# Kernel optimization log

Measured on AMD Instinct MI355X. Metric: run time of the kernel, lower is better.

Reference implementation:

```python
import jax, jax.numpy as jnp
from jax import lax
import numpy as np

B, C_IN, D, H, W = 1, 8, 48, 256, 320
BC = 8  # base_channels
DN = ('NCHW', 'OIHW', 'NCHW')


def setup_inputs() -> dict:
    key = jax.random.key(0)
    ks = iter(jax.random.split(key, 64))
    inp = {"volume_variance": jax.random.normal(next(ks), (B, C_IN, D, H, W), jnp.float32)}
    def add(name, o, i):
        inp[name + "_w"] = jax.random.normal(next(ks), (o, i, 3, 3), jnp.float32) * 0.1
        inp[name + "_b"] = jnp.zeros((o,), jnp.float32)
    add("conv1", 2 * BC, C_IN); add("conv2", 4 * BC, 2 * BC); add("conv3", 8 * BC, 4 * BC)
    add("up3", 4 * BC, 8 * BC); add("up2", 2 * BC, 4 * BC); add("up1", BC, 2 * BC)
    add("out", 1, BC)
    add("g1_gate", 2 * BC, C_IN + BC); add("g1_cand", BC, C_IN + BC)
    add("g2_gate", 4 * BC, 4 * BC); add("g2_cand", 2 * BC, 4 * BC)
    add("g3_gate", 8 * BC, 8 * BC); add("g3_cand", 4 * BC, 8 * BC)
    add("g4_gate", 16 * BC, 16 * BC); add("g4_cand", 8 * BC, 16 * BC)
    return inp


def _conv(x, w, b, stride=1):
    # Conv2d(k=3, padding=1)
    y = lax.conv_general_dilated(x, w, (stride, stride), [(1, 1), (1, 1)], dimension_numbers=DN)
    return y + b[None, :, None, None]


def _convT(x, w, b):
    # PyTorch ConvTranspose2d(k=3, s=2, p=1, output_padding=1) as an input-dilated conv
    y = lax.conv_general_dilated(x, w, (1, 1), [(1, 2), (1, 2)], lhs_dilation=(2, 2),
                                 dimension_numbers=DN)
    return y + b[None, :, None, None]


def _gru(x, h, wg, bg, wc, bc):
    # ConvGRUCell2: fused reset/update gates, tanh candidate, convex combine
    gates = jax.nn.sigmoid(_conv(jnp.concatenate([x, h], 1), wg, bg))
    r, u = jnp.split(gates, 2, 1)
    c = jnp.tanh(_conv(jnp.concatenate([x, r * h], 1), wc, bc))
    return u * h + (1.0 - u) * c


def reference(volume_variance, conv1_w, conv1_b, conv2_w, conv2_b, conv3_w, conv3_b,
              up3_w, up3_b, up2_w, up2_b, up1_w, up1_b, out_w, out_b,
              g1_gate_w, g1_gate_b, g1_cand_w, g1_cand_b,
              g2_gate_w, g2_gate_b, g2_cand_w, g2_cand_b,
              g3_gate_w, g3_gate_b, g3_cand_w, g3_cand_b,
              g4_gate_w, g4_gate_b, g4_cand_w, g4_cand_b):
    def step(carry, cost):
        s1, s2, s3, s4 = carry
        nc = -cost                                            # [B, C_IN, H, W]
        c1 = jax.nn.relu(_conv(nc, conv1_w, conv1_b, 2))      # [B, 2BC, H/2, W/2]
        c2 = jax.nn.relu(_conv(c1, conv2_w, conv2_b, 2))      # [B, 4BC, H/4, W/4]
        c3 = jax.nn.relu(_conv(c2, conv3_w, conv3_b, 2))      # [B, 8BC, H/8, W/8]
        r4 = _gru(c3, s4, g4_gate_w, g4_gate_b, g4_cand_w, g4_cand_b)
        u3 = jax.nn.relu(_convT(r4, up3_w, up3_b))            # [B, 4BC, H/4, W/4]
        r3 = _gru(c2, s3, g3_gate_w, g3_gate_b, g3_cand_w, g3_cand_b)
        u2 = jax.nn.relu(_convT(u3 + r3, up2_w, up2_b))       # [B, 2BC, H/2, W/2]
        r2 = _gru(c1, s2, g2_gate_w, g2_gate_b, g2_cand_w, g2_cand_b)
        u1 = jax.nn.relu(_convT(u2 + r2, up1_w, up1_b))       # [B, BC, H, W]
        r1 = _gru(nc, s1, g1_gate_w, g1_gate_b, g1_cand_w, g1_cand_b)
        # ConvTranspose2d(k=3, s=1, p=1, op=0) is exactly a 3x3 same-pad conv (reparam'd weight)
        reg = _conv(u1 + r1, out_w, out_b)                    # [B, 1, H, W]
        return (r1, r2, r3, r4), reg[:, 0]
    costs = jnp.moveaxis(volume_variance, 2, 0)               # [D, B, C_IN, H, W]
    init = (jnp.zeros((B, BC, H, W), jnp.float32),
            jnp.zeros((B, 2 * BC, H // 2, W // 2), jnp.float32),
            jnp.zeros((B, 4 * BC, H // 4, W // 4), jnp.float32),
            jnp.zeros((B, 8 * BC, H // 8, W // 8), jnp.float32))
    _, outs = lax.scan(step, init, costs)                     # outs: [D, B, H, W]
    return jnp.moveaxis(outs, 0, 1)                           # [B, D, H, W]
```

## Files before the change

kernel.cpp:

```cpp
#include <hip/hip_runtime.h>
#include <math.h>

namespace {

constexpr int H0 = 256, W0 = 320, H1 = 128, W1 = 160, H2 = 64, W2 = 80, H3 = 32, W3 = 40;
constexpr int HW0 = H0 * W0, HW1 = H1 * W1, HW2 = H2 * W2, HW3 = H3 * W3;
constexpr int DEPTH = 48;
constexpr int NCS = DEPTH * HW0;

template <int CX, int CH, int COUT, int TX, int TY, int OCPT, int CHUNK,
          bool NEGX, bool CAND, int ZC>
__device__ __forceinline__ void gru_conv(
    int bx, int by, int zg, int H, int W,
    const float* __restrict__ x, int xcs,
    const float* __restrict__ h, const float* __restrict__ rg,
    const float* __restrict__ w, const float* __restrict__ bias,
    float* __restrict__ out, float* lds) {
  constexpr int CIN = CX + CH, IH = TY + 2, IW = TX + 2;
  constexpr int NPX = TX * TY, SUBS = 256 / NPX, NOCG = COUT / OCPT;
  constexpr int GPER = NOCG / ZC, NITER = GPER / SUBS;
  static_assert(NITER * SUBS == GPER && GPER * ZC == NOCG, "cfg");
  static_assert(CHUNK * IH * IW <= 6400, "lds");
  const int x0 = bx * TX, y0 = by * TY, HW = H * W, tid = threadIdx.x;
  const int px = tid % NPX, sub = tid / NPX, tx = px % TX, ty = px / TX;
  const int gbase = zg * GPER + sub;
  float acc[NITER][OCPT];
#pragma unroll
  for (int it = 0; it < NITER; it++) {
    const int g = gbase + it * SUBS;
#pragma unroll
    for (int j = 0; j < OCPT; j++) acc[it][j] = bias[g * OCPT + j];
  }
  for (int c0 = 0; c0 < CIN; c0 += CHUNK) {
    __syncthreads();
    for (int idx = tid; idx < CHUNK * IH * IW; idx += 256) {
      int cc = idx / (IH * IW), r = idx % (IH * IW), yy = r / IW, xx = r % IW;
      int gy = y0 + yy - 1, gx = x0 + xx - 1, c = c0 + cc;
      float v = 0.f;
      if ((unsigned)gy < (unsigned)H && (unsigned)gx < (unsigned)W) {
        if (c < CX) {
          v = x[(size_t)c * xcs + gy * W + gx];
          if (NEGX) v = -v;
        } else {
          int p = (c - CX) * HW + gy * W + gx;
          v = h[p];
          if (CAND) v *= rg[p];
        }
      }
      lds[idx] = v;
    }
    __syncthreads();
    for (int c = 0; c < CHUNK; c++) {
      float v[9];
      const float* lp = lds + (c * IH + ty) * IW + tx;
#pragma unroll
      for (int ky = 0; ky < 3; ky++)
#pragma unroll
        for (int kx = 0; kx < 3; kx++) v[ky * 3 + kx] = lp[ky * IW + kx];
#pragma unroll
      for (int it = 0; it < NITER; it++) {
        const int g = __builtin_amdgcn_readfirstlane(gbase + it * SUBS);
        const float* wc = w + ((size_t)(g * OCPT) * CIN + (c0 + c)) * 9;
#pragma unroll
        for (int j = 0; j < OCPT; j++)
#pragma unroll
          for (int k = 0; k < 9; k++)
            acc[it][j] = fmaf(v[k], wc[(size_t)j * CIN * 9 + k], acc[it][j]);
      }
    }
  }
  const int opix = (y0 + ty) * W + x0 + tx;
#pragma unroll
  for (int it = 0; it < NITER; it++) {
    const int g = gbase + it * SUBS;
#pragma unroll
    for (int j = 0; j < OCPT; j++) {
      const int oc = g * OCPT + j;
      float a = acc[it][j];
      if (!CAND) {
        out[oc * HW + opix] = 1.f / (1.f + expf(-a));
      } else {
        float cd = tanhf(a);
        float u = rg[(CH + oc) * HW + opix];
        float hv = h[oc * HW + opix];
        out[oc * HW + opix] = u * hv + (1.f - u) * cd;
      }
    }
  }
}

struct GruArgs {
  const float* x; int xcs;
  const float* c1; const float* c2; const float* c3;
  const float* h1; const float* h2; const float* h3; const float* h4;
  const float* g1; const float* g2; const float* g3; const float* g4;
  const float* w1; const float* b1; const float* w2; const float* b2;
  const float* w3; const float* b3; const float* w4; const float* b4;
  float* o1; float* o2; float* o3; float* o4;
};

__global__ __launch_bounds__(256) void gates_k(GruArgs a) {
  __shared__ float lds[6400];
  const int b = blockIdx.x;
  if (b < 320) {
    gru_conv<8, 8, 16, 16, 16, 8, 16, true, false, 1>(
        b % 20, b / 20, 0, H0, W0, a.x, a.xcs, a.h1, nullptr, a.w1, a.b1, a.o1, lds);
  } else if (b < 640) {
    int l = b - 320;
    gru_conv<16, 16, 32, 16, 8, 8, 32, false, false, 2>(
        l % 10, (l / 10) % 16, l / 160, H1, W1, a.c1, HW1, a.h2, nullptr, a.w2, a.b2, a.o2, lds);
  } else if (b < 800) {
    int l = b - 640;
    gru_conv<32, 32, 64, 8, 8, 8, 64, false, false, 2>(
        l % 10, (l / 10) % 8, l / 80, H2, W2, a.c2, HW2, a.h3, nullptr, a.w3, a.b3, a.o3, lds);
  } else {
    int l = b - 800;
    gru_conv<64, 64, 128, 8, 8, 4, 64, false, false, 8>(
        l % 5, (l / 5) % 4, l / 20, H3, W3, a.c3, HW3, a.h4, nullptr, a.w4, a.b4, a.o4, lds);
  }
}

__global__ __launch_bounds__(256) void cands_k(GruArgs a) {
  __shared__ float lds[6400];
  const int b = blockIdx.x;
  if (b < 320) {
    gru_conv<8, 8, 8, 16, 16, 8, 16, true, true, 1>(
        b % 20, b / 20, 0, H0, W0, a.x, a.xcs, a.h1, a.g1, a.w1, a.b1, a.o1, lds);
  } else if (b < 480) {
    int l = b - 320;
    gru_conv<16, 16, 16, 16, 8, 8, 32, false, true, 1>(
        l % 10, l / 10, 0, H1, W1, a.c1, HW1, a.h2, a.g2, a.w2, a.b2, a.o2, lds);
  } else if (b < 560) {
    int l = b - 480;
    gru_conv<32, 32, 32, 8, 8, 8, 64, false, true, 1>(
        l % 10, l / 10, 0, H2, W2, a.c2, HW2, a.h3, a.g3, a.w3, a.b3, a.o3, lds);
  } else {
    int l = b - 560;
    gru_conv<64, 64, 64, 8, 8, 4, 64, false, true, 4>(
        l % 5, (l / 5) % 4, l / 20, H3, W3, a.c3, HW3, a.h4, a.g4, a.w4, a.b4, a.o4, lds);
  }
}

template <int CIN, int COUT, int TX, int TY, int OCPT, int ZC, bool NEG>
__global__ __launch_bounds__(256) void enc_k(
    const float* __restrict__ in, int inCS, size_t inTS, int inSlots,
    const float* __restrict__ w, const float* __restrict__ bias,
    float* __restrict__ out, size_t outTS, int outSlots,
    int inH, int inW, int outH, int outW, int t0) {
  constexpr int IH = 2 * TY + 1, IW = 2 * TX + 1;
  constexpr int NPX = TX * TY, SUBS = 256 / NPX, NOCG = COUT / OCPT;
  constexpr int GPER = NOCG / ZC, NITER = GPER / SUBS;
  static_assert(NITER * SUBS == GPER, "cfg");
  __shared__ float lds[CIN * IH * IW];
  const int z = blockIdx.z, tt = t0 + z / ZC, zg = z % ZC;
  const float* inp = in + (size_t)(tt % inSlots) * inTS;
  float* outp = out + (size_t)(tt % outSlots) * outTS;
  const int x0 = blockIdx.x * TX, y0 = blockIdx.y * TY;
  const int ix0 = 2 * x0 - 1, iy0 = 2 * y0 - 1, tid = threadIdx.x;
  for (int idx = tid; idx < CIN * IH * IW; idx += 256) {
    int c = idx / (IH * IW), r = idx % (IH * IW), yy = r / IW, xx = r % IW;
    int gy = iy0 + yy, gx = ix0 + xx;
    float v = 0.f;
    if ((unsigned)gy < (unsigned)inH && (unsigned)gx < (unsigned)inW)
      v = inp[(size_t)c * inCS + gy * inW + gx];
    lds[idx] = NEG ? -v : v;
  }
  __syncthreads();
  const int px = tid % NPX, sub = tid / NPX, tx = px % TX, ty = px / TX;
  const int gbase = zg * GPER + sub;
  float acc[NITER][OCPT];
#pragma unroll
  for (int it = 0; it < NITER; it++) {
    const int g = gbase + it * SUBS;
#pragma unroll
    for (int j = 0; j < OCPT; j++) acc[it][j] = bias[g * OCPT + j];
  }
  for (int c = 0; c < CIN; c++) {
    float v[9];
    const float* lp = lds + (c * IH + 2 * ty) * IW + 2 * tx;
#pragma unroll
    for (int ky = 0; ky < 3; ky++)
#pragma unroll
      for (int kx = 0; kx < 3; kx++) v[ky * 3 + kx] = lp[ky * IW + kx];
#pragma unroll
    for (int it = 0; it < NITER; it++) {
      const int g = __builtin_amdgcn_readfirstlane(gbase + it * SUBS);
      const float* wc = w + ((size_t)(g * OCPT) * CIN + c) * 9;
#pragma unroll
      for (int j = 0; j < OCPT; j++)
#pragma unroll
        for (int k = 0; k < 9; k++)
          acc[it][j] = fmaf(v[k], wc[(size_t)j * CIN * 9 + k], acc[it][j]);
    }
  }
  const int ox = x0 + tx, oy = y0 + ty;
#pragma unroll
  for (int it = 0; it < NITER; it++) {
    const int g = gbase + it * SUBS;
#pragma unroll
    for (int j = 0; j < OCPT; j++)
      outp[((size_t)(g * OCPT + j) * outH + oy) * outW + ox] = fmaxf(acc[it][j], 0.f);
  }
}

template <int CIN, int COUT, int OCPT, int ZC, bool SUM2>
__global__ __launch_bounds__(256) void convT_b_k(
    const float* __restrict__ inA, size_t aTS, int aSlots,
    const float* __restrict__ inB, size_t bTS, int bSlots,
    const float* __restrict__ w, const float* __restrict__ bias,
    float* __restrict__ out, size_t oTS, int oSlots,
    int inH, int inW, int t0) {
  __shared__ float lds[CIN * 81];
  const int z = blockIdx.z, tt = t0 + z / ZC, zg = z % ZC;
  const float* A = inA + (size_t)(tt % aSlots) * aTS;
  const float* Bp = inB + (size_t)(tt % bSlots) * bTS;
  float* outp = out + (size_t)(tt % oSlots) * oTS;
  const int x0 = blockIdx.x * 16, y0 = blockIdx.y * 16, ix0 = x0 / 2, iy0 = y0 / 2;
  const int HWin = inH * inW, tid = threadIdx.x;
  for (int idx = tid; idx < CIN * 81; idx += 256) {
    int c = idx / 81, r = idx % 81, yy = r / 9, xx = r % 9;
    int gy = iy0 + yy, gx = ix0 + xx;
    float v = 0.f;
    if (gy < inH && gx < inW) {
      int p = c * HWin + gy * inW + gx;
      v = A[p];
      if (SUM2) v += Bp[p];
    }
    lds[idx] = v;
  }
  __syncthreads();
  constexpr int NOCG = COUT / OCPT, GPER = NOCG / ZC, SUBS = 4, NITER = GPER / SUBS;
  static_assert(NITER * SUBS == GPER, "cfg");
  const int q = tid % 64, sub = tid / 64, qx = q % 8, qy = q / 8;
  const int outW = 2 * inW, oy = y0 + 2 * qy, ox = x0 + 2 * qx;
  const int gbase = zg * GPER + sub;
  float a00[NITER][OCPT], a01[NITER][OCPT], a10[NITER][OCPT], a11[NITER][OCPT];
#pragma unroll
  for (int it = 0; it < NITER; it++) {
    const int g = gbase + it * SUBS;
#pragma unroll
    for (int j = 0; j < OCPT; j++) {
      float bb = bias[g * OCPT + j];
      a00[it][j] = bb; a01[it][j] = bb; a10[it][j] = bb; a11[it][j] = bb;
    }
  }
  for (int c = 0; c < CIN; c++) {
    const float* ip = lds + c * 81 + qy * 9 + qx;
    const float v00 = ip[0], v01 = ip[1], v10 = ip[9], v11 = ip[10];
#pragma unroll
    for (int it = 0; it < NITER; it++) {
      const int g = __builtin_amdgcn_readfirstlane(gbase + it * SUBS);
      const float* wg = w + ((size_t)(g * OCPT) * CIN + c) * 9;
#pragma unroll
      for (int j = 0; j < OCPT; j++) {
        const float* wc = wg + (size_t)j * CIN * 9;
        a00[it][j] = fmaf(wc[4], v00, a00[it][j]);
        a01[it][j] = fmaf(wc[3], v00, a01[it][j]);
        a01[it][j] = fmaf(wc[5], v01, a01[it][j]);
        a10[it][j] = fmaf(wc[1], v00, a10[it][j]);
        a10[it][j] = fmaf(wc[7], v10, a10[it][j]);
        a11[it][j] = fmaf(wc[0], v00, a11[it][j]);
        a11[it][j] = fmaf(wc[2], v01, a11[it][j]);
        a11[it][j] = fmaf(wc[6], v10, a11[it][j]);
        a11[it][j] = fmaf(wc[8], v11, a11[it][j]);
      }
    }
  }
  const int base = oy * outW + ox;
#pragma unroll
  for (int it = 0; it < NITER; it++) {
    const int g = gbase + it * SUBS;
#pragma unroll
    for (int j = 0; j < OCPT; j++) {
      float* op = outp + (size_t)(g * OCPT + j) * (4 * HWin);
      op[base] = fmaxf(a00[it][j], 0.f);
      op[base + 1] = fmaxf(a01[it][j], 0.f);
      op[base + outW] = fmaxf(a10[it][j], 0.f);
      op[base + outW + 1] = fmaxf(a11[it][j], 0.f);
    }
  }
}

__global__ __launch_bounds__(256) void up1out_k(
    const float* __restrict__ u2, size_t u2TS, int u2S,
    const float* __restrict__ r2, size_t r2TS, int r2S,
    const float* __restrict__ r1, size_t r1TS, int r1S,
    const float* __restrict__ wT, const float* __restrict__ bT,
    const float* __restrict__ wo, const float* __restrict__ bo,
    float* __restrict__ dout, int t0) {
  __shared__ float ins[16 * 121];
  __shared__ float u1h[8 * 400];
  const int t = t0 + blockIdx.z;
  const float* U = u2 + (size_t)(t % u2S) * u2TS;
  const float* R2 = r2 + (size_t)(t % r2S) * r2TS;
  const float* R1 = r1 + (size_t)(t % r1S) * r1TS;
  const int x0 = blockIdx.x * 16, y0 = blockIdx.y * 16;
  const int ix0 = x0 / 2 - 1, iy0 = y0 / 2 - 1, tid = threadIdx.x;
  for (int idx = tid; idx < 16 * 121; idx += 256) {
    int c = idx / 121, r = idx % 121, yy = r / 11, xx = r % 11;
    int gy = iy0 + yy, gx = ix0 + xx;
    float v = 0.f;
    if ((unsigned)gy < (unsigned)H1 && (unsigned)gx < (unsigned)W1) {
      int p = c * HW1 + gy * W1 + gx;
      v = U[p] + R2[p];
    }
    ins[idx] = v;
  }
  __syncthreads();
  for (int u = tid; u < 800; u += 256) {
    int ch = u / 100, qq = u % 100, qy = qq / 10, qx = qq % 10;
    float bb = bT[ch];
    float a00 = bb, a01 = bb, a10 = bb, a11 = bb;
    const float* wb = wT + (size_t)ch * 16 * 9;
    for (int ic = 0; ic < 16; ic++) {
      const float* wc = wb + ic * 9;
      const float* ip = ins + ic * 121 + qy * 11 + qx;
      float v00 = ip[0], v01 = ip[1], v10 = ip[11], v11 = ip[12];
      a00 = fmaf(wc[4], v00, a00);
      a01 = fmaf(wc[3], v00, a01); a01 = fmaf(wc[5], v01, a01);
      a10 = fmaf(wc[1], v00, a10); a10 = fmaf(wc[7], v10, a10);
      a11 = fmaf(wc[0], v00, a11); a11 = fmaf(wc[2], v01, a11);
      a11 = fmaf(wc[6], v10, a11); a11 = fmaf(wc[8], v11, a11);
    }
    float* up = u1h + ch * 400 + (2 * qy) * 20 + 2 * qx;
    up[0] = fmaxf(a00, 0.f);  up[1] = fmaxf(a01, 0.f);
    up[20] = fmaxf(a10, 0.f); up[21] = fmaxf(a11, 0.f);
  }
  __syncthreads();
  for (int idx = tid; idx < 8 * 400; idx += 256) {
    int c = idx / 400, r = idx % 400, hy = r / 20, hx = r % 20;
    int gy = y0 - 2 + hy, gx = x0 - 2 + hx;
    if ((unsigned)gy < (unsigned)H0 && (unsigned)gx < (unsigned)W0)
      u1h[idx] += R1[c * HW0 + gy * W0 + gx];
    else
      u1h[idx] = 0.f;
  }
  __syncthreads();
  const int tx = tid % 16, ty = tid / 16;
  float acc = bo[0];
  for (int c = 0; c < 8; c++) {
    const float* up = u1h + c * 400 + (ty + 1) * 20 + tx + 1;
#pragma unroll
    for (int ky = 0; ky < 3; ky++)
#pragma unroll
      for (int kx = 0; kx < 3; kx++)
        acc = fmaf(up[ky * 20 + kx], wo[c * 9 + ky * 3 + kx], acc);
  }
  dout[(size_t)t * HW0 + (y0 + ty) * W0 + x0 + tx] = acc;
}

}

extern "C" void kernel_launch(void* const* d_in, const int* in_sizes, int n_in,
                              void* d_out, int out_size, void* d_ws, size_t ws_size,
                              hipStream_t stream) {
  const float* vol = (const float*)d_in[0];
  const float* c1w = (const float*)d_in[1];  const float* c1b = (const float*)d_in[2];
  const float* c2w = (const float*)d_in[3];  const float* c2b = (const float*)d_in[4];
  const float* c3w = (const float*)d_in[5];  const float* c3b = (const float*)d_in[6];
  const float* u3w = (const float*)d_in[7];  const float* u3b = (const float*)d_in[8];
  const float* u2w = (const float*)d_in[9];  const float* u2b = (const float*)d_in[10];
  const float* u1w = (const float*)d_in[11]; const float* u1b = (const float*)d_in[12];
  const float* ow  = (const float*)d_in[13]; const float* ob  = (const float*)d_in[14];
  const float* g1gw = (const float*)d_in[15]; const float* g1gb = (const float*)d_in[16];
  const float* g1cw = (const float*)d_in[17]; const float* g1cb = (const float*)d_in[18];
  const float* g2gw = (const float*)d_in[19]; const float* g2gb = (const float*)d_in[20];
  const float* g2cw = (const float*)d_in[21]; const float* g2cb = (const float*)d_in[22];
  const float* g3gw = (const float*)d_in[23]; const float* g3gb = (const float*)d_in[24];
  const float* g3cw = (const float*)d_in[25]; const float* g3cb = (const float*)d_in[26];
  const float* g4gw = (const float*)d_in[27]; const float* g4gb = (const float*)d_in[28];
  const float* g4cw = (const float*)d_in[29]; const float* g4cb = (const float*)d_in[30];
  float* dout = (float*)d_out;
  (void)in_sizes; (void)n_in; (void)out_size;

  const size_t r1Sz = 8 * HW0, r2Sz = 16 * HW1, r3Sz = 32 * HW2, r4Sz = 64 * HW3;
  const size_t c1Sz = 16 * HW1, c2Sz = 32 * HW2, c3Sz = 64 * HW3;
  const size_t g1Sz = 16 * HW0, g2Sz = 32 * HW1, g3Sz = 64 * HW2, g4Sz = 128 * HW3;
  const size_t ZB = 8 * HW0;
  const size_t rTot = r1Sz + r2Sz + r3Sz + r4Sz;
  const size_t cTot = c1Sz + c2Sz + c3Sz;
  const size_t gTot = g1Sz + g2Sz + g3Sz + g4Sz;
  const size_t uTot = 32 * HW2 + 16 * HW1;
  const size_t needA = (ZB + 48 * rTot + 48 * cTot + gTot) * sizeof(float);
  const size_t needB = (ZB + 2 * rTot + 48 * cTot + gTot + uTot) * sizeof(float);
  const int tier = ws_size >= needA ? 0 : (ws_size >= needB ? 1 : 2);
  const int TR = (tier == 0) ? 48 : 2;
  const int TC = (tier == 2) ? 1 : 48;

  float* ws = (float*)d_ws;
  size_t off = 0;
  auto alloc = [&](size_t n) { float* p = ws + off; off += n; return p; };
  float* zb = alloc(ZB);
  float* r1 = alloc((size_t)TR * r1Sz); float* r2 = alloc((size_t)TR * r2Sz);
  float* r3 = alloc((size_t)TR * r3Sz); float* r4 = alloc((size_t)TR * r4Sz);
  float* g1 = alloc(g1Sz); float* g2 = alloc(g2Sz);
  float* g3 = alloc(g3Sz); float* g4 = alloc(g4Sz);
  float* c1a = alloc((size_t)TC * c1Sz);
  float* c2a = alloc((size_t)TC * c2Sz);
  float* c3a = alloc((size_t)TC * c3Sz);
  float *u3a, *u2a;
  if (tier == 0) {
    u3a = c1a;
    u2a = c1a + 48 * (32 * HW2);
  } else {
    u3a = alloc(32 * HW2);
    u2a = alloc(16 * HW1);
  }

  hipMemsetAsync(zb, 0, ZB * sizeof(float), stream);

  const int TD = (tier == 0) ? 48 : 1;
  if (tier < 2) {
    enc_k<8, 16, 16, 16, 8, 1, true><<<dim3(10, 8, 48), 256, 0, stream>>>(
        vol, NCS, (size_t)HW0, 48, c1w, c1b, c1a, c1Sz, 48, H0, W0, H1, W1, 0);
    enc_k<16, 32, 16, 8, 8, 1, false><<<dim3(5, 8, 48), 256, 0, stream>>>(
        c1a, HW1, c1Sz, 48, c2w, c2b, c2a, c2Sz, 48, H1, W1, H2, W2, 0);
    enc_k<32, 64, 8, 8, 8, 2, false><<<dim3(5, 4, 96), 256, 0, stream>>>(
        c2a, HW2, c2Sz, 48, c3w, c3b, c3a, c3Sz, 48, H2, W2, H3, W3, 0);
  }

  for (int t = 0; t < DEPTH; t++) {
    if (tier == 2) {
      enc_k<8, 16, 16, 16, 8, 1, true><<<dim3(10, 8, 1), 256, 0, stream>>>(
          vol, NCS, (size_t)HW0, 48, c1w, c1b, c1a, c1Sz, 1, H0, W0, H1, W1, t);
      enc_k<16, 32, 16, 8, 8, 1, false><<<dim3(5, 8, 1), 256, 0, stream>>>(
          c1a, HW1, c1Sz, 1, c2w, c2b, c2a, c2Sz, 1, H1, W1, H2, W2, t);
      enc_k<32, 64, 8, 8, 8, 2, false><<<dim3(5, 4, 2), 256, 0, stream>>>(
          c2a, HW2, c2Sz, 1, c3w, c3b, c3a, c3Sz, 1, H2, W2, H3, W3, t);
    }
    const float* x0p = vol + (size_t)t * HW0;
    const float* h1p = t ? r1 + (size_t)((t - 1) % TR) * r1Sz : zb;
    const float* h2p = t ? r2 + (size_t)((t - 1) % TR) * r2Sz : zb;
    const float* h3p = t ? r3 + (size_t)((t - 1) % TR) * r3Sz : zb;
    const float* h4p = t ? r4 + (size_t)((t - 1) % TR) * r4Sz : zb;
    const float* c1p = c1a + (size_t)(t % TC) * c1Sz;
    const float* c2p = c2a + (size_t)(t % TC) * c2Sz;
    const float* c3p = c3a + (size_t)(t % TC) * c3Sz;
    float* o1p = r1 + (size_t)(t % TR) * r1Sz;
    float* o2p = r2 + (size_t)(t % TR) * r2Sz;
    float* o3p = r3 + (size_t)(t % TR) * r3Sz;
    float* o4p = r4 + (size_t)(t % TR) * r4Sz;

    GruArgs ga{x0p, NCS, c1p, c2p, c3p, h1p, h2p, h3p, h4p,
               nullptr, nullptr, nullptr, nullptr,
               g1gw, g1gb, g2gw, g2gb, g3gw, g3gb, g4gw, g4gb,
               g1, g2, g3, g4};
    gates_k<<<dim3(960), 256, 0, stream>>>(ga);
    GruArgs ca{x0p, NCS, c1p, c2p, c3p, h1p, h2p, h3p, h4p,
               g1, g2, g3, g4,
               g1cw, g1cb, g2cw, g2cb, g3cw, g3cb, g4cw, g4cb,
               o1p, o2p, o3p, o4p};
    cands_k<<<dim3(640), 256, 0, stream>>>(ca);

    if (tier > 0) {
      convT_b_k<64, 32, 4, 2, false><<<dim3(5, 4, 2), 256, 0, stream>>>(
          r4, r4Sz, TR, r4, 0, 1, u3w, u3b, u3a, (size_t)32 * HW2, 1, H3, W3, t);
      convT_b_k<32, 16, 4, 1, true><<<dim3(10, 8, 1), 256, 0, stream>>>(
          u3a, (size_t)32 * HW2, 1, r3, r3Sz, TR, u2w, u2b, u2a, (size_t)16 * HW1, 1,
          H2, W2, t);
      up1out_k<<<dim3(20, 16, 1), 256, 0, stream>>>(
          u2a, (size_t)16 * HW1, 1, r2, r2Sz, TR, r1, r1Sz, TR,
          u1w, u1b, ow, ob, dout, t);
    }
  }

  if (tier == 0) {
    convT_b_k<64, 32, 4, 2, false><<<dim3(5, 4, 2 * TD), 256, 0, stream>>>(
        r4, r4Sz, 48, r4, 0, 1, u3w, u3b, u3a, (size_t)32 * HW2, 48, H3, W3, 0);
    convT_b_k<32, 16, 4, 1, true><<<dim3(10, 8, TD), 256, 0, stream>>>(
        u3a, (size_t)32 * HW2, 48, r3, r3Sz, 48, u2w, u2b, u2a, (size_t)16 * HW1, 48,
        H2, W2, 0);
    up1out_k<<<dim3(20, 16, TD), 256, 0, stream>>>(
        u2a, (size_t)16 * HW1, 48, r2, r2Sz, 48, r1, r1Sz, 48,
        u1w, u1b, ow, ob, dout, 0);
  }
}
```

Before: 9.164 ms.

## Rework conv kernels with 2x2 register tiles, transposed weights and XCD block remap

Rewrites the GRU, encoder and transposed-conv kernels so each thread computes a 2x2 output quad over several output channels, loading a 4x4 (or 5x5) LDS patch and reusing each weight across four pixels. Weights are pre-transposed once per call to [in][out][9] layout so that consecutive output channels are contiguous. Grids are flattened to 1D and block indices are remapped so neighbouring tiles land on the same XCD for L2 locality. Tile, chunk and channel-group sizes are retuned at the same time. Occupancy and LDS use change, and there is one extra small transpose launch per call.

```diff
diff --git a/kernel.cpp b/kernel.cpp
--- a/kernel.cpp
+++ b/kernel.cpp
@@ -8,41 +8,47 @@
 constexpr int DEPTH = 48;
 constexpr int NCS = DEPTH * HW0;
 
-template <int CX, int CH, int COUT, int TX, int TY, int OCPT, int CHUNK,
-          bool NEGX, bool CAND, int ZC>
-__device__ __forceinline__ void gru_conv(
+__device__ __forceinline__ int xcd_remap(int b, int n) {
+  const int q = n >> 3, r = n & 7, xcd = b & 7, i = b >> 3;
+  return (xcd < r ? xcd * (q + 1) : r * (q + 1) + (xcd - r) * q) + i;
+}
+
+template <int CX, int CH, int COUT, int QX, int QY, int OCPT, int CHUNK,
+          bool NEGX, bool CAND, int ZC, bool UNIF>
+__device__ __forceinline__ void gru_conv_q(
     int bx, int by, int zg, int H, int W,
     const float* __restrict__ x, int xcs,
     const float* __restrict__ h, const float* __restrict__ rg,
-    const float* __restrict__ w, const float* __restrict__ bias,
+    const float* __restrict__ wT, const float* __restrict__ bias,
     float* __restrict__ out, float* lds) {
-  constexpr int CIN = CX + CH, IH = TY + 2, IW = TX + 2;
-  constexpr int NPX = TX * TY, SUBS = 256 / NPX, NOCG = COUT / OCPT;
-  constexpr int GPER = NOCG / ZC, NITER = GPER / SUBS;
-  static_assert(NITER * SUBS == GPER && GPER * ZC == NOCG, "cfg");
+  constexpr int CIN = CX + CH, TPX = 2 * QX, TPY = 2 * QY;
+  constexpr int IW = TPX + 2, IH = TPY + 2;
+  constexpr int NQ = QX * QY, SUBS = 256 / NQ;
+  static_assert(SUBS * OCPT * ZC == COUT, "cfg");
   static_assert(CHUNK * IH * IW <= 6400, "lds");
-  const int x0 = bx * TX, y0 = by * TY, HW = H * W, tid = threadIdx.x;
-  const int px = tid % NPX, sub = tid / NPX, tx = px % TX, ty = px / TX;
-  const int gbase = zg * GPER + sub;
-  float acc[NITER][OCPT];
-#pragma unroll
-  for (int it = 0; it < NITER; it++) {
-    const int g = gbase + it * SUBS;
-#pragma unroll
-    for (int j = 0; j < OCPT; j++) acc[it][j] = bias[g * OCPT + j];
+  const int x0 = bx * TPX, y0 = by * TPY, HW = H * W, tid = threadIdx.x;
+  const int q = tid % NQ, sub = tid / NQ;
+  const int qx = q % QX, qy = q / QX;
+  int ocb = zg * (COUT / ZC) + sub * OCPT;
+  if (UNIF) ocb = __builtin_amdgcn_readfirstlane(ocb);
+  float acc[OCPT][4];
+#pragma unroll
+  for (int j = 0; j < OCPT; j++) {
+    const float bb = bias[ocb + j];
+    acc[j][0] = bb; acc[j][1] = bb; acc[j][2] = bb; acc[j][3] = bb;
   }
   for (int c0 = 0; c0 < CIN; c0 += CHUNK) {
     __syncthreads();
     for (int idx = tid; idx < CHUNK * IH * IW; idx += 256) {
-      int cc = idx / (IH * IW), r = idx % (IH * IW), yy = r / IW, xx = r % IW;
-      int gy = y0 + yy - 1, gx = x0 + xx - 1, c = c0 + cc;
+      const int cc = idx / (IH * IW), rr = idx % (IH * IW), yy = rr / IW, xx = rr % IW;
+      const int gy = y0 + yy - 1, gx = x0 + xx - 1, c = c0 + cc;
       float v = 0.f;
       if ((unsigned)gy < (unsigned)H && (unsigned)gx < (unsigned)W) {
         if (c < CX) {
           v = x[(size_t)c * xcs + gy * W + gx];
           if (NEGX) v = -v;
         } else {
-          int p = (c - CX) * HW + gy * W + gx;
+          const int p = (c - CX) * HW + gy * W + gx;
           v = h[p];
           if (CAND) v *= rg[p];
         }
@@ -51,46 +57,54 @@
     }
     __syncthreads();
     for (int c = 0; c < CHUNK; c++) {
-      float v[9];
-      const float* lp = lds + (c * IH + ty) * IW + tx;
-#pragma unroll
-      for (int ky = 0; ky < 3; ky++)
-#pragma unroll
-        for (int kx = 0; kx < 3; kx++) v[ky * 3 + kx] = lp[ky * IW + kx];
-#pragma unroll
-      for (int it = 0; it < NITER; it++) {
-        const int g = __builtin_amdgcn_readfirstlane(gbase + it * SUBS);
-        const float* wc = w + ((size_t)(g * OCPT) * CIN + (c0 + c)) * 9;
-#pragma unroll
-        for (int j = 0; j < OCPT; j++)
-#pragma unroll
-          for (int k = 0; k < 9; k++)
-            acc[it][j] = fmaf(v[k], wc[(size_t)j * CIN * 9 + k], acc[it][j]);
-      }
-    }
-  }
-  const int opix = (y0 + ty) * W + x0 + tx;
-#pragma unroll
-  for (int it = 0; it < NITER; it++) {
-    const int g = gbase + it * SUBS;
-#pragma unroll
-    for (int j = 0; j < OCPT; j++) {
-      const int oc = g * OCPT + j;
-      float a = acc[it][j];
-      if (!CAND) {
-        out[oc * HW + opix] = 1.f / (1.f + expf(-a));
-      } else {
-        float cd = tanhf(a);
-        float u = rg[(CH + oc) * HW + opix];
-        float hv = h[oc * HW + opix];
-        out[oc * HW + opix] = u * hv + (1.f - u) * cd;
-      }
-    }
+      float p[4][4];
+      const float* lp = lds + (c * IH + 2 * qy) * IW + 2 * qx;
+#pragma unroll
+      for (int r = 0; r < 4; r++) {
+        const float2 a = *(const float2*)(lp + r * IW);
+        const float2 b = *(const float2*)(lp + r * IW + 2);
+        p[r][0] = a.x; p[r][1] = a.y; p[r][2] = b.x; p[r][3] = b.y;
+      }
+#pragma unroll
+      for (int j = 0; j < OCPT; j++) {
+        const float* wc = wT + ((size_t)(c0 + c) * COUT + ocb + j) * 9;
+#pragma unroll
+        for (int ky = 0; ky < 3; ky++)
+#pragma unroll
+          for (int kx = 0; kx < 3; kx++) {
+            const float wv = wc[ky * 3 + kx];
+            acc[j][0] = fmaf(p[ky][kx],         wv, acc[j][0]);
+            acc[j][1] = fmaf(p[ky][kx + 1],     wv, acc[j][1]);
+            acc[j][2] = fmaf(p[ky + 1][kx],     wv, acc[j][2]);
+            acc[j][3] = fmaf(p[ky + 1][kx + 1], wv, acc[j][3]);
+          }
+      }
+    }
+  }
+  const int ox = x0 + 2 * qx, oy = y0 + 2 * qy;
+#pragma unroll
+  for (int j = 0; j < OCPT; j++) {
+    const int oc = ocb + j;
+#pragma unroll
+    for (int py = 0; py < 2; py++)
+#pragma unroll
+      for (int px = 0; px < 2; px++) {
+        const int opix = (oy + py) * W + ox + px;
+        const float a = acc[j][py * 2 + px];
+        if (!CAND) {
+          out[oc * HW + opix] = 1.f / (1.f + expf(-a));
+        } else {
+          const float cd = tanhf(a);
+          const float u = rg[(CH + oc) * HW + opix];
+          const float hv = h[oc * HW + opix];
+          out[oc * HW + opix] = u * hv + (1.f - u) * cd;
+        }
+      }
   }
 }
 
 struct GruArgs {
-  const float* x; int xcs;
+  const float* x;
   const float* c1; const float* c2; const float* c3;
   const float* h1; const float* h2; const float* h3; const float* h4;
   const float* g1; const float* g2; const float* g3; const float* g4;
@@ -100,184 +114,206 @@
 };
 
 __global__ __launch_bounds__(256) void gates_k(GruArgs a) {
-  __shared__ float lds[6400];
-  const int b = blockIdx.x;
+  __shared__ __align__(16) float lds[6400];
+  const int b = xcd_remap(blockIdx.x, 1120);
   if (b < 320) {
-    gru_conv<8, 8, 16, 16, 16, 8, 16, true, false, 1>(
-        b % 20, b / 20, 0, H0, W0, a.x, a.xcs, a.h1, nullptr, a.w1, a.b1, a.o1, lds);
+    gru_conv_q<8, 8, 16, 8, 8, 4, 16, true, false, 1, true>(
+        b % 20, b / 20, 0, H0, W0, a.x, NCS, a.h1, nullptr, a.w1, a.b1, a.o1, lds);
   } else if (b < 640) {
-    int l = b - 320;
-    gru_conv<16, 16, 32, 16, 8, 8, 32, false, false, 2>(
-        l % 10, (l / 10) % 16, l / 160, H1, W1, a.c1, HW1, a.h2, nullptr, a.w2, a.b2, a.o2, lds);
-  } else if (b < 800) {
-    int l = b - 640;
-    gru_conv<32, 32, 64, 8, 8, 8, 64, false, false, 2>(
+    const int l = b - 320;
+    gru_conv_q<16, 16, 32, 8, 8, 2, 16, false, false, 4, true>(
+        l % 10, (l / 10) % 8, l / 80, H1, W1, a.c1, HW1, a.h2, nullptr, a.w2, a.b2, a.o2, lds);
+  } else if (b < 960) {
+    const int l = b - 640;
+    gru_conv_q<32, 32, 64, 4, 4, 1, 32, false, false, 4, false>(
         l % 10, (l / 10) % 8, l / 80, H2, W2, a.c2, HW2, a.h3, nullptr, a.w3, a.b3, a.o3, lds);
   } else {
-    int l = b - 800;
-    gru_conv<64, 64, 128, 8, 8, 4, 64, false, false, 8>(
+    const int l = b - 960;
+    gru_conv_q<64, 64, 128, 4, 4, 1, 64, false, false, 8, false>(
         l % 5, (l / 5) % 4, l / 20, H3, W3, a.c3, HW3, a.h4, nullptr, a.w4, a.b4, a.o4, lds);
   }
 }
 
 __global__ __launch_bounds__(256) void cands_k(GruArgs a) {
-  __shared__ float lds[6400];
-  const int b = blockIdx.x;
+  __shared__ __align__(16) float lds[6400];
+  const int b = xcd_remap(blockIdx.x, 720);
   if (b < 320) {
-    gru_conv<8, 8, 8, 16, 16, 8, 16, true, true, 1>(
-        b % 20, b / 20, 0, H0, W0, a.x, a.xcs, a.h1, a.g1, a.w1, a.b1, a.o1, lds);
+    gru_conv_q<8, 8, 8, 8, 8, 2, 16, true, true, 1, true>(
+        b % 20, b / 20, 0, H0, W0, a.x, NCS, a.h1, a.g1, a.w1, a.b1, a.o1, lds);
   } else if (b < 480) {
-    int l = b - 320;
-    gru_conv<16, 16, 16, 16, 8, 8, 32, false, true, 1>(
-        l % 10, l / 10, 0, H1, W1, a.c1, HW1, a.h2, a.g2, a.w2, a.b2, a.o2, lds);
-  } else if (b < 560) {
-    int l = b - 480;
-    gru_conv<32, 32, 32, 8, 8, 8, 64, false, true, 1>(
-        l % 10, l / 10, 0, H2, W2, a.c2, HW2, a.h3, a.g3, a.w3, a.b3, a.o3, lds);
+    const int l = b - 320;
+    gru_conv_q<16, 16, 16, 8, 8, 2, 16, false, true, 2, true>(
+        l % 10, (l / 10) % 8, l / 80, H1, W1, a.c1, HW1, a.h2, a.g2, a.w2, a.b2, a.o2, lds);
+  } else if (b < 640) {
+    const int l = b - 480;
+    gru_conv_q<32, 32, 32, 4, 4, 1, 32, false, true, 2, false>(
+        l % 10, (l / 10) % 8, l / 80, H2, W2, a.c2, HW2, a.h3, a.g3, a.w3, a.b3, a.o3, lds);
   } else {
-    int l = b - 560;
-    gru_conv<64, 64, 64, 8, 8, 4, 64, false, true, 4>(
+    const int l = b - 640;
+    gru_conv_q<64, 64, 64, 4, 4, 1, 64, false, true, 4, false>(
         l % 5, (l / 5) % 4, l / 20, H3, W3, a.c3, HW3, a.h4, a.g4, a.w4, a.b4, a.o4, lds);
   }
 }
 
-template <int CIN, int COUT, int TX, int TY, int OCPT, int ZC, bool NEG>
-__global__ __launch_bounds__(256) void enc_k(
+template <int CIN, int COUT, int QX, int QY, int OCPT, int CHUNK, bool NEG,
+          int INH, int INW, int ONH, int ONW, bool UNIF>
+__global__ __launch_bounds__(256) void enc_q_k(
     const float* __restrict__ in, int inCS, size_t inTS, int inSlots,
-    const float* __restrict__ w, const float* __restrict__ bias,
-    float* __restrict__ out, size_t outTS, int outSlots,
-    int inH, int inW, int outH, int outW, int t0) {
-  constexpr int IH = 2 * TY + 1, IW = 2 * TX + 1;
-  constexpr int NPX = TX * TY, SUBS = 256 / NPX, NOCG = COUT / OCPT;
-  constexpr int GPER = NOCG / ZC, NITER = GPER / SUBS;
-  static_assert(NITER * SUBS == GPER, "cfg");
-  __shared__ float lds[CIN * IH * IW];
-  const int z = blockIdx.z, tt = t0 + z / ZC, zg = z % ZC;
+    const float* __restrict__ wT, const float* __restrict__ bias,
+    float* __restrict__ out, size_t outTS, int outSlots, int t0, int n) {
+  constexpr int TPX = 2 * QX, TPY = 2 * QY, IW = 2 * TPX + 1, IH = 2 * TPY + 1;
+  constexpr int SX = ONW / TPX, SY = ONH / TPY, NQ = QX * QY, SUBS = 256 / NQ;
+  static_assert(SUBS * OCPT == COUT, "cfg");
+  __shared__ float lds[CHUNK * IH * IW];
+  const int lb = xcd_remap(blockIdx.x, n);
+  const int z = lb / (SX * SY), rr = lb % (SX * SY);
+  const int bx = rr % SX, by = rr / SX, tt = t0 + z;
   const float* inp = in + (size_t)(tt % inSlots) * inTS;
   float* outp = out + (size_t)(tt % outSlots) * outTS;
-  const int x0 = blockIdx.x * TX, y0 = blockIdx.y * TY;
+  const int x0 = bx * TPX, y0 = by * TPY;
   const int ix0 = 2 * x0 - 1, iy0 = 2 * y0 - 1, tid = threadIdx.x;
-  for (int idx = tid; idx < CIN * IH * IW; idx += 256) {
-    int c = idx / (IH * IW), r = idx % (IH * IW), yy = r / IW, xx = r % IW;
-    int gy = iy0 + yy, gx = ix0 + xx;
+  const int q = tid % NQ, sub = tid / NQ, qx = q % QX, qy = q / QX;
+  int ocb = sub * OCPT;
+  if (UNIF) ocb = __builtin_amdgcn_readfirstlane(ocb);
+  float acc[OCPT][4];
+#pragma unroll
+  for (int j = 0; j < OCPT; j++) {
+    const float bb = bias[ocb + j];
+    acc[j][0] = bb; acc[j][1] = bb; acc[j][2] = bb; acc[j][3] = bb;
+  }
+  for (int c0 = 0; c0 < CIN; c0 += CHUNK) {
+    __syncthreads();
+    for (int idx = tid; idx < CHUNK * IH * IW; idx += 256) {
+      const int cc = idx / (IH * IW), r2 = idx % (IH * IW), yy = r2 / IW, xx = r2 % IW;
+      const int gy = iy0 + yy, gx = ix0 + xx;
+      float v = 0.f;
+      if ((unsigned)gy < (unsigned)INH && (unsigned)gx < (unsigned)INW)
+        v = inp[(size_t)(c0 + cc) * inCS + gy * INW + gx];
+      lds[idx] = NEG ? -v : v;
+    }
+    __syncthreads();
+    for (int c = 0; c < CHUNK; c++) {
+      float p[5][5];
+      const float* lp = lds + (c * IH + 4 * qy) * IW + 4 * qx;
+#pragma unroll
+      for (int r = 0; r < 5; r++)
+#pragma unroll
+        for (int s = 0; s < 5; s++) p[r][s] = lp[r * IW + s];
+#pragma unroll
+      for (int j = 0; j < OCPT; j++) {
+        const float* wc = wT + ((size_t)(c0 + c) * COUT + ocb + j) * 9;
+#pragma unroll
+        for (int ky = 0; ky < 3; ky++)
+#pragma unroll
+          for (int kx = 0; kx < 3; kx++) {
+            const float wv = wc[ky * 3 + kx];
+            acc[j][0] = fmaf(p[ky][kx],         wv, acc[j][0]);
+            acc[j][1] = fmaf(p[ky][kx + 2],     wv, acc[j][1]);
+            acc[j][2] = fmaf(p[ky + 2][kx],     wv, acc[j][2]);
+            acc[j][3] = fmaf(p[ky + 2][kx + 2], wv, acc[j][3]);
+          }
+      }
+    }
+  }
+  const int ox = x0 + 2 * qx, oy = y0 + 2 * qy;
+#pragma unroll
+  for (int j = 0; j < OCPT; j++)
+#pragma unroll
+    for (int py = 0; py < 2; py++)
+#pragma unroll
+      for (int px = 0; px < 2; px++)
+        outp[((size_t)(ocb + j) * ONH + oy + py) * ONW + ox + px] =
+            fmaxf(acc[j][py * 2 + px], 0.f);
+}
+
+template <int CIN, int COUT, int OCPT, bool SUM2, int INH, int INW>
+__global__ __launch_bounds__(256) void convT_q_k(
+    const float* __restrict__ A, size_t aTS, int aSlots,
+    const float* __restrict__ B, size_t bTS, int bSlots,
+    const float* __restrict__ wT, const float* __restrict__ bias,
+    float* __restrict__ out, size_t oTS, int oSlots, int t0, int n) {
+  constexpr int SX = (2 * INW) / 16, SY = (2 * INH) / 16, SUBS = 16;
+  static_assert(SUBS * OCPT == COUT, "cfg");
+  __shared__ float lds[CIN * 81];
+  const int lb = xcd_remap(blockIdx.x, n);
+  const int z = lb / (SX * SY), rr = lb % (SX * SY);
+  const int bx = rr % SX, by = rr / SX, tt = t0 + z;
+  const float* Ap = A + (size_t)(tt % aSlots) * aTS;
+  const float* Bp = B + (size_t)(tt % bSlots) * bTS;
+  float* outp = out + (size_t)(tt % oSlots) * oTS;
+  const int x0 = bx * 16, y0 = by * 16, ix0 = x0 / 2, iy0 = y0 / 2;
+  const int HWin = INH * INW, tid = threadIdx.x;
+  for (int idx = tid; idx < CIN * 81; idx += 256) {
+    const int c = idx / 81, r = idx % 81, yy = r / 9, xx = r % 9;
+    const int gy = iy0 + yy, gx = ix0 + xx;
     float v = 0.f;
-    if ((unsigned)gy < (unsigned)inH && (unsigned)gx < (unsigned)inW)
-      v = inp[(size_t)c * inCS + gy * inW + gx];
-    lds[idx] = NEG ? -v : v;
+    if (gy < INH && gx < INW) {
+      const int p = c * HWin + gy * INW + gx;
+      v = Ap[p];
+      if (SUM2) v += Bp[p];
+    }
+    lds[idx] = v;
   }
   __syncthreads();
-  const int px = tid % NPX, sub = tid / NPX, tx = px % TX, ty = px / TX;
-  const int gbase = zg * GPER + sub;
-  float acc[NITER][OCPT];
-#pragma unroll
-  for (int it = 0; it < NITER; it++) {
-    const int g = gbase + it * SUBS;
-#pragma unroll
-    for (int j = 0; j < OCPT; j++) acc[it][j] = bias[g * OCPT + j];
+  const int cb = tid % 16, sub = tid / 16;
+  const int cbx = cb % 4, cby = cb / 4;
+  const int ocb = sub * OCPT;
+  float a00[OCPT][4], a01[OCPT][4], a10[OCPT][4], a11[OCPT][4];
+#pragma unroll
+  for (int j = 0; j < OCPT; j++) {
+    const float bb = bias[ocb + j];
+#pragma unroll
+    for (int qi = 0; qi < 4; qi++) {
+      a00[j][qi] = bb; a01[j][qi] = bb; a10[j][qi] = bb; a11[j][qi] = bb;
+    }
   }
   for (int c = 0; c < CIN; c++) {
-    float v[9];
-    const float* lp = lds + (c * IH + 2 * ty) * IW + 2 * tx;
-#pragma unroll
-    for (int ky = 0; ky < 3; ky++)
-#pragma unroll
-      for (int kx = 0; kx < 3; kx++) v[ky * 3 + kx] = lp[ky * IW + kx];
-#pragma unroll
-    for (int it = 0; it < NITER; it++) {
-      const int g = __builtin_amdgcn_readfirstlane(gbase + it * SUBS);
-      const float* wc = w + ((size_t)(g * OCPT) * CIN + c) * 9;
-#pragma unroll
-      for (int j = 0; j < OCPT; j++)
-#pragma unroll
-        for (int k = 0; k < 9; k++)
-          acc[it][j] = fmaf(v[k], wc[(size_t)j * CIN * 9 + k], acc[it][j]);
-    }
-  }
-  const int ox = x0 + tx, oy = y0 + ty;
-#pragma unroll
-  for (int it = 0; it < NITER; it++) {
-    const int g = gbase + it * SUBS;
-#pragma unroll
-    for (int j = 0; j < OCPT; j++)
-      outp[((size_t)(g * OCPT + j) * outH + oy) * outW + ox] = fmaxf(acc[it][j], 0.f);
-  }
-}
-
-template <int CIN, int COUT, int OCPT, int ZC, bool SUM2>
-__global__ __launch_bounds__(256) void convT_b_k(
-    const float* __restrict__ inA, size_t aTS, int aSlots,
-    const float* __restrict__ inB, size_t bTS, int bSlots,
-    const float* __restrict__ w, const float* __restrict__ bias,
-    float* __restrict__ out, size_t oTS, int oSlots,
-    int inH, int inW, int t0) {
-  __shared__ float lds[CIN * 81];
-  const int z = blockIdx.z, tt = t0 + z / ZC, zg = z % ZC;
-  const float* A = inA + (size_t)(tt % aSlots) * aTS;
-  const float* Bp = inB + (size_t)(tt % bSlots) * bTS;
-  float* outp = out + (size_t)(tt % oSlots) * oTS;
-  const int x0 = blockIdx.x * 16, y0 = blockIdx.y * 16, ix0 = x0 / 2, iy0 = y0 / 2;
-  const int HWin = inH * inW, tid = threadIdx.x;
-  for (int idx = tid; idx < CIN * 81; idx += 256) {
-    int c = idx / 81, r = idx % 81, yy = r / 9, xx = r % 9;
-    int gy = iy0 + yy, gx = ix0 + xx;
-    float v = 0.f;
-    if (gy < inH && gx < inW) {
-      int p = c * HWin + gy * inW + gx;
-      v = A[p];
-      if (SUM2) v += Bp[p];
-    }
-    lds[idx] = v;
-  }
-  __syncthreads();
-  constexpr int NOCG = COUT / OCPT, GPER = NOCG / ZC, SUBS = 4, NITER = GPER / SUBS;
-  static_assert(NITER * SUBS == GPER, "cfg");
-  const int q = tid % 64, sub = tid / 64, qx = q % 8, qy = q / 8;
-  const int outW = 2 * inW, oy = y0 + 2 * qy, ox = x0 + 2 * qx;
-  const int gbase = zg * GPER + sub;
-  float a00[NITER][OCPT], a01[NITER][OCPT], a10[NITER][OCPT], a11[NITER][OCPT];
-#pragma unroll
-  for (int it = 0; it < NITER; it++) {
-    const int g = gbase + it * SUBS;
+    float p[3][3];
+    const float* ip = lds + c * 81 + (2 * cby) * 9 + 2 * cbx;
+#pragma unroll
+    for (int r = 0; r < 3; r++)
+#pragma unroll
+      for (int s = 0; s < 3; s++) p[r][s] = ip[r * 9 + s];
 #pragma unroll
     for (int j = 0; j < OCPT; j++) {
-      float bb = bias[g * OCPT + j];
-      a00[it][j] = bb; a01[it][j] = bb; a10[it][j] = bb; a11[it][j] = bb;
-    }
-  }
-  for (int c = 0; c < CIN; c++) {
-    const float* ip = lds + c * 81 + qy * 9 + qx;
-    const float v00 = ip[0], v01 = ip[1], v10 = ip[9], v11 = ip[10];
-#pragma unroll
-    for (int it = 0; it < NITER; it++) {
-      const int g = __builtin_amdgcn_readfirstlane(gbase + it * SUBS);
-      const float* wg = w + ((size_t)(g * OCPT) * CIN + c) * 9;
-#pragma unroll
-      for (int j = 0; j < OCPT; j++) {
-        const float* wc = wg + (size_t)j * CIN * 9;
-        a00[it][j] = fmaf(wc[4], v00, a00[it][j]);
-        a01[it][j] = fmaf(wc[3], v00, a01[it][j]);
-        a01[it][j] = fmaf(wc[5], v01, a01[it][j]);
-        a10[it][j] = fmaf(wc[1], v00, a10[it][j]);
-        a10[it][j] = fmaf(wc[7], v10, a10[it][j]);
-        a11[it][j] = fmaf(wc[0], v00, a11[it][j]);
-        a11[it][j] = fmaf(wc[2], v01, a11[it][j]);
-        a11[it][j] = fmaf(wc[6], v10, a11[it][j]);
-        a11[it][j] = fmaf(wc[8], v11, a11[it][j]);
-      }
-    }
-  }
-  const int base = oy * outW + ox;
-#pragma unroll
-  for (int it = 0; it < NITER; it++) {
-    const int g = gbase + it * SUBS;
-#pragma unroll
-    for (int j = 0; j < OCPT; j++) {
-      float* op = outp + (size_t)(g * OCPT + j) * (4 * HWin);
-      op[base] = fmaxf(a00[it][j], 0.f);
-      op[base + 1] = fmaxf(a01[it][j], 0.f);
-      op[base + outW] = fmaxf(a10[it][j], 0.f);
-      op[base + outW + 1] = fmaxf(a11[it][j], 0.f);
-    }
+      const float* wc = wT + ((size_t)c * COUT + ocb + j) * 9;
+      const float w0 = wc[0], w1 = wc[1], w2 = wc[2], w3 = wc[3], w4 = wc[4];
+      const float w5 = wc[5], w6 = wc[6], w7 = wc[7], w8 = wc[8];
+#pragma unroll
+      for (int dy = 0; dy < 2; dy++)
+#pragma unroll
+        for (int dx = 0; dx < 2; dx++) {
+          const int qi = dy * 2 + dx;
+          const float v00 = p[dy][dx], v01 = p[dy][dx + 1];
+          const float v10 = p[dy + 1][dx], v11 = p[dy + 1][dx + 1];
+          a00[j][qi] = fmaf(w4, v00, a00[j][qi]);
+          a01[j][qi] = fmaf(w3, v00, a01[j][qi]);
+          a01[j][qi] = fmaf(w5, v01, a01[j][qi]);
+          a10[j][qi] = fmaf(w1, v00, a10[j][qi]);
+          a10[j][qi] = fmaf(w7, v10, a10[j][qi]);
+          a11[j][qi] = fmaf(w0, v00, a11[j][qi]);
+          a11[j][qi] = fmaf(w2, v01, a11[j][qi]);
+          a11[j][qi] = fmaf(w6, v10, a11[j][qi]);
+          a11[j][qi] = fmaf(w8, v11, a11[j][qi]);
+        }
+    }
+  }
+  const int outW = 2 * INW;
+#pragma unroll
+  for (int j = 0; j < OCPT; j++) {
+    float* op = outp + (size_t)(ocb + j) * (4 * HWin);
+#pragma unroll
+    for (int dy = 0; dy < 2; dy++)
+#pragma unroll
+      for (int dx = 0; dx < 2; dx++) {
+        const int qi = dy * 2 + dx;
+        const int ox = x0 + 2 * (2 * cbx + dx), oy = y0 + 2 * (2 * cby + dy);
+        const int base = oy * outW + ox;
+        op[base] = fmaxf(a00[j][qi], 0.f);
+        op[base + 1] = fmaxf(a01[j][qi], 0.f);
+        op[base + outW] = fmaxf(a10[j][qi], 0.f);
+        op[base + outW + 1] = fmaxf(a11[j][qi], 0.f);
+      }
   }
 }
 
@@ -285,51 +321,76 @@
     const float* __restrict__ u2, size_t u2TS, int u2S,
     const float* __restrict__ r2, size_t r2TS, int r2S,
     const float* __restrict__ r1, size_t r1TS, int r1S,
-    const float* __restrict__ wT, const float* __restrict__ bT,
+    const float* __restrict__ wTu1, const float* __restrict__ bT,
     const float* __restrict__ wo, const float* __restrict__ bo,
-    float* __restrict__ dout, int t0) {
+    float* __restrict__ dout, int t0, int n) {
   __shared__ float ins[16 * 121];
   __shared__ float u1h[8 * 400];
-  const int t = t0 + blockIdx.z;
+  const int lb = xcd_remap(blockIdx.x, n);
+  const int z = lb / 320, rr = lb % 320, bx = rr % 20, by = rr / 20;
+  const int t = t0 + z;
   const float* U = u2 + (size_t)(t % u2S) * u2TS;
   const float* R2 = r2 + (size_t)(t % r2S) * r2TS;
   const float* R1 = r1 + (size_t)(t % r1S) * r1TS;
-  const int x0 = blockIdx.x * 16, y0 = blockIdx.y * 16;
+  const int x0 = bx * 16, y0 = by * 16;
   const int ix0 = x0 / 2 - 1, iy0 = y0 / 2 - 1, tid = threadIdx.x;
   for (int idx = tid; idx < 16 * 121; idx += 256) {
-    int c = idx / 121, r = idx % 121, yy = r / 11, xx = r % 11;
-    int gy = iy0 + yy, gx = ix0 + xx;
+    const int c = idx / 121, r = idx % 121, yy = r / 11, xx = r % 11;
+    const int gy = iy0 + yy, gx = ix0 + xx;
     float v = 0.f;
     if ((unsigned)gy < (unsigned)H1 && (unsigned)gx < (unsigned)W1) {
-      int p = c * HW1 + gy * W1 + gx;
+      const int p = c * HW1 + gy * W1 + gx;
       v = U[p] + R2[p];
     }
     ins[idx] = v;
   }
   __syncthreads();
-  for (int u = tid; u < 800; u += 256) {
-    int ch = u / 100, qq = u % 100, qy = qq / 10, qx = qq % 10;
-    float bb = bT[ch];
-    float a00 = bb, a01 = bb, a10 = bb, a11 = bb;
-    const float* wb = wT + (size_t)ch * 16 * 9;
+  if (tid < 200) {
+    const int ch = tid / 25, cb = tid % 25, cbx = cb % 5, cby = cb / 5;
+    const float bb = bT[ch];
+    float A0[4], A1[4], A2[4], A3[4];
+#pragma unroll
+    for (int qi = 0; qi < 4; qi++) { A0[qi] = bb; A1[qi] = bb; A2[qi] = bb; A3[qi] = bb; }
     for (int ic = 0; ic < 16; ic++) {
-      const float* wc = wb + ic * 9;
-      const float* ip = ins + ic * 121 + qy * 11 + qx;
-      float v00 = ip[0], v01 = ip[1], v10 = ip[11], v11 = ip[12];
-      a00 = fmaf(wc[4], v00, a00);
-      a01 = fmaf(wc[3], v00, a01); a01 = fmaf(wc[5], v01, a01);
-      a10 = fmaf(wc[1], v00, a10); a10 = fmaf(wc[7], v10, a10);
-      a11 = fmaf(wc[0], v00, a11); a11 = fmaf(wc[2], v01, a11);
-      a11 = fmaf(wc[6], v10, a11); a11 = fmaf(wc[8], v11, a11);
-    }
-    float* up = u1h + ch * 400 + (2 * qy) * 20 + 2 * qx;
-    up[0] = fmaxf(a00, 0.f);  up[1] = fmaxf(a01, 0.f);
-    up[20] = fmaxf(a10, 0.f); up[21] = fmaxf(a11, 0.f);
+      float p[3][3];
+      const float* ip = ins + ic * 121 + (2 * cby) * 11 + 2 * cbx;
+#pragma unroll
+      for (int r = 0; r < 3; r++)
+#pragma unroll
+        for (int s = 0; s < 3; s++) p[r][s] = ip[r * 11 + s];
+      const float* wc = wTu1 + ((size_t)ic * 8 + ch) * 9;
+      const float w0 = wc[0], w1 = wc[1], w2 = wc[2], w3 = wc[3], w4 = wc[4];
+      const float w5 = wc[5], w6 = wc[6], w7 = wc[7], w8 = wc[8];
+#pragma unroll
+      for (int dy = 0; dy < 2; dy++)
+#pragma unroll
+        for (int dx = 0; dx < 2; dx++) {
+          const int qi = dy * 2 + dx;
+          const float v00 = p[dy][dx], v01 = p[dy][dx + 1];
+          const float v10 = p[dy + 1][dx], v11 = p[dy + 1][dx + 1];
+          A0[qi] = fmaf(w4, v00, A0[qi]);
+          A1[qi] = fmaf(w3, v00, A1[qi]); A1[qi] = fmaf(w5, v01, A1[qi]);
+          A2[qi] = fmaf(w1, v00, A2[qi]); A2[qi] = fmaf(w7, v10, A2[qi]);
+          A3[qi] = fmaf(w0, v00, A3[qi]); A3[qi] = fmaf(w2, v01, A3[qi]);
+          A3[qi] = fmaf(w6, v10, A3[qi]); A3[qi] = fmaf(w8, v11, A3[qi]);
+        }
+    }
+#pragma unroll
+    for (int dy = 0; dy < 2; dy++)
+#pragma unroll
+      for (int dx = 0; dx < 2; dx++) {
+        const int qi = dy * 2 + dx;
+        float* up = u1h + ch * 400 + (2 * (2 * cby + dy)) * 20 + 2 * (2 * cbx + dx);
+        up[0] = fmaxf(A0[qi], 0.f);
+        up[1] = fmaxf(A1[qi], 0.f);
+        up[20] = fmaxf(A2[qi], 0.f);
+        up[21] = fmaxf(A3[qi], 0.f);
+      }
   }
   __syncthreads();
   for (int idx = tid; idx < 8 * 400; idx += 256) {
-    int c = idx / 400, r = idx % 400, hy = r / 20, hx = r % 20;
-    int gy = y0 - 2 + hy, gx = x0 - 2 + hx;
+    const int c = idx / 400, r = idx % 400, hy = r / 20, hx = r % 20;
+    const int gy = y0 - 2 + hy, gx = x0 - 2 + hx;
     if ((unsigned)gy < (unsigned)H0 && (unsigned)gx < (unsigned)W0)
       u1h[idx] += R1[c * HW0 + gy * W0 + gx];
     else
@@ -347,6 +408,19 @@
         acc = fmaf(up[ky * 20 + kx], wo[c * 9 + ky * 3 + kx], acc);
   }
   dout[(size_t)t * HW0 + (y0 + ty) * W0 + x0 + tx] = acc;
+}
+
+struct WT { const float* s; float* d; int O; int I; };
+struct WTab { WT t[14]; };
+__global__ __launch_bounds__(256) void wtrans_k(WTab a) {
+  for (int ti = 0; ti < 14; ti++) {
+    const int O = a.t[ti].O, I = a.t[ti].I, nn = O * I * 9;
+    for (int idx = blockIdx.x * 256 + threadIdx.x; idx < nn; idx += gridDim.x * 256) {
+      const int k = idx % 9, oi = idx / 9;
+      const int i = oi % I, o = oi / I;
+      a.t[ti].d[((size_t)i * O + o) * 9 + k] = a.t[ti].s[idx];
+    }
+  }
 }
 
 }
@@ -381,15 +455,22 @@
   const size_t cTot = c1Sz + c2Sz + c3Sz;
   const size_t gTot = g1Sz + g2Sz + g3Sz + g4Sz;
   const size_t uTot = 32 * HW2 + 16 * HW1;
-  const size_t needA = (ZB + 48 * rTot + 48 * cTot + gTot) * sizeof(float);
-  const size_t needB = (ZB + 2 * rTot + 48 * cTot + gTot + uTot) * sizeof(float);
+  const size_t wTot = 342144;
+  const size_t needA = (wTot + ZB + 48 * rTot + 48 * cTot + gTot) * sizeof(float);
+  const size_t needB = (wTot + ZB + 2 * rTot + 48 * cTot + gTot + uTot) * sizeof(float);
   const int tier = ws_size >= needA ? 0 : (ws_size >= needB ? 1 : 2);
   const int TR = (tier == 0) ? 48 : 2;
   const int TC = (tier == 2) ? 1 : 48;
 
   float* ws = (float*)d_ws;
   size_t off = 0;
-  auto alloc = [&](size_t n) { float* p = ws + off; off += n; return p; };
+  auto alloc = [&](size_t nn) { float* p = ws + off; off += nn; return p; };
+  float* wt_c1 = alloc(1152);   float* wt_c2 = alloc(4608);  float* wt_c3 = alloc(18432);
+  float* wt_u3 = alloc(18432);  float* wt_u2 = alloc(4608);  float* wt_u1 = alloc(1152);
+  float* wt_g1g = alloc(2304);  float* wt_g1c = alloc(1152);
+  float* wt_g2g = alloc(9216);  float* wt_g2c = alloc(4608);
+  float* wt_g3g = alloc(36864); float* wt_g3c = alloc(18432);
+  float* wt_g4g = alloc(147456); float* wt_g4c = alloc(73728);
   float* zb = alloc(ZB);
   float* r1 = alloc((size_t)TR * r1Sz); float* r2 = alloc((size_t)TR * r2Sz);
   float* r3 = alloc((size_t)TR * r3Sz); float* r4 = alloc((size_t)TR * r4Sz);
@@ -407,26 +488,38 @@
     u2a = alloc(16 * HW1);
   }
 
+  WTab wt{{{c1w, wt_c1, 16, 8},   {c2w, wt_c2, 32, 16},  {c3w, wt_c3, 64, 32},
+           {u3w, wt_u3, 32, 64},  {u2w, wt_u2, 16, 32},  {u1w, wt_u1, 8, 16},
+           {g1gw, wt_g1g, 16, 16}, {g1cw, wt_g1c, 8, 16},
+           {g2gw, wt_g2g, 32, 32}, {g2cw, wt_g2c, 16, 32},
+           {g3gw, wt_g3g, 64, 64}, {g3cw, wt_g3c, 32, 64},
+           {g4gw, wt_g4g, 128, 128}, {g4cw, wt_g4c, 64, 128}}};
+  wtrans_k<<<dim3(128), 256, 0, stream>>>(wt);
   hipMemsetAsync(zb, 0, ZB * sizeof(float), stream);
 
-  const int TD = (tier == 0) ? 48 : 1;
   if (tier < 2) {
-    enc_k<8, 16, 16, 16, 8, 1, true><<<dim3(10, 8, 48), 256, 0, stream>>>(
-        vol, NCS, (size_t)HW0, 48, c1w, c1b, c1a, c1Sz, 48, H0, W0, H1, W1, 0);
-    enc_k<16, 32, 16, 8, 8, 1, false><<<dim3(5, 8, 48), 256, 0, stream>>>(
-        c1a, HW1, c1Sz, 48, c2w, c2b, c2a, c2Sz, 48, H1, W1, H2, W2, 0);
-    enc_k<32, 64, 8, 8, 8, 2, false><<<dim3(5, 4, 96), 256, 0, stream>>>(
-        c2a, HW2, c2Sz, 48, c3w, c3b, c3a, c3Sz, 48, H2, W2, H3, W3, 0);
+    enc_q_k<8, 16, 8, 8, 4, 8, true, 256, 320, 128, 160, true>
+        <<<dim3(3840), 256, 0, stream>>>(vol, NCS, (size_t)HW0, 48, wt_c1, c1b,
+                                         c1a, c1Sz, 48, 0, 3840);
+    enc_q_k<16, 32, 8, 8, 8, 8, false, 128, 160, 64, 80, true>
+        <<<dim3(960), 256, 0, stream>>>(c1a, HW1, c1Sz, 48, wt_c2, c2b,
+                                        c2a, c2Sz, 48, 0, 960);
+    enc_q_k<32, 64, 4, 4, 4, 16, false, 64, 80, 32, 40, false>
+        <<<dim3(960), 256, 0, stream>>>(c2a, HW2, c2Sz, 48, wt_c3, c3b,
+                                        c3a, c3Sz, 48, 0, 960);
   }
 
   for (int t = 0; t < DEPTH; t++) {
     if (tier == 2) {
-      enc_k<8, 16, 16, 16, 8, 1, true><<<dim3(10, 8, 1), 256, 0, stream>>>(
-          vol, NCS, (size_t)HW0, 48, c1w, c1b, c1a, c1Sz, 1, H0, W0, H1, W1, t);
-      enc_k<16, 32, 16, 8, 8, 1, false><<<dim3(5, 8, 1), 256, 0, stream>>>(
-          c1a, HW1, c1Sz, 1, c2w, c2b, c2a, c2Sz, 1, H1, W1, H2, W2, t);
-      enc_k<32, 64, 8, 8, 8, 2, false><<<dim3(5, 4, 2), 256, 0, stream>>>(
-          c2a, HW2, c2Sz, 1, c3w, c3b, c3a, c3Sz, 1, H2, W2, H3, W3, t);
+      enc_q_k<8, 16, 8, 8, 4, 8, true, 256, 320, 128, 160, true>
+          <<<dim3(80), 256, 0, stream>>>(vol, NCS, (size_t)HW0, 48, wt_c1, c1b,
+                                         c1a, c1Sz, 1, t, 80);
+      enc_q_k<16, 32, 8, 8, 8, 8, false, 128, 160, 64, 80, true>
+          <<<dim3(20), 256, 0, stream>>>(c1a, HW1, c1Sz, 1, wt_c2, c2b,
+                                         c2a, c2Sz, 1, t, 20);
+      enc_q_k<32, 64, 4, 4, 4, 16, false, 64, 80, 32, 40, false>
+          <<<dim3(20), 256, 0, stream>>>(c2a, HW2, c2Sz, 1, wt_c3, c3b,
+                                         c3a, c3Sz, 1, t, 20);
     }
     const float* x0p = vol + (size_t)t * HW0;
     const float* h1p = t ? r1 + (size_t)((t - 1) % TR) * r1Sz : zb;
@@ -441,37 +534,39 @@
     float* o3p = r3 + (size_t)(t % TR) * r3Sz;
     float* o4p = r4 + (size_t)(t % TR) * r4Sz;
 
-    GruArgs ga{x0p, NCS, c1p, c2p, c3p, h1p, h2p, h3p, h4p,
+    GruArgs ga{x0p, c1p, c2p, c3p, h1p, h2p, h3p, h4p,
                nullptr, nullptr, nullptr, nullptr,
-               g1gw, g1gb, g2gw, g2gb, g3gw, g3gb, g4gw, g4gb,
+               wt_g1g, g1gb, wt_g2g, g2gb, wt_g3g, g3gb, wt_g4g, g4gb,
                g1, g2, g3, g4};
-    gates_k<<<dim3(960), 256, 0, stream>>>(ga);
-    GruArgs ca{x0p, NCS, c1p, c2p, c3p, h1p, h2p, h3p, h4p,
+    gates_k<<<dim3(1120), 256, 0, stream>>>(ga);
+    GruArgs ca{x0p, c1p, c2p, c3p, h1p, h2p, h3p, h4p,
                g1, g2, g3, g4,
-               g1cw, g1cb, g2cw, g2cb, g3cw, g3cb, g4cw, g4cb,
+               wt_g1c, g1cb, wt_g2c, g2cb, wt_g3c, g3cb, wt_g4c, g4cb,
                o1p, o2p, o3p, o4p};
-    cands_k<<<dim3(640), 256, 0, stream>>>(ca);
+    cands_k<<<dim3(720), 256, 0, stream>>>(ca);
 
     if (tier > 0) {
-      convT_b_k<64, 32, 4, 2, false><<<dim3(5, 4, 2), 256, 0, stream>>>(
-          r4, r4Sz, TR, r4, 0, 1, u3w, u3b, u3a, (size_t)32 * HW2, 1, H3, W3, t);
-      convT_b_k<32, 16, 4, 1, true><<<dim3(10, 8, 1), 256, 0, stream>>>(
-          u3a, (size_t)32 * HW2, 1, r3, r3Sz, TR, u2w, u2b, u2a, (size_t)16 * HW1, 1,
-          H2, W2, t);
-      up1out_k<<<dim3(20, 16, 1), 256, 0, stream>>>(
+      convT_q_k<64, 32, 2, false, 32, 40>
+          <<<dim3(20), 256, 0, stream>>>(r4, r4Sz, TR, r4, 0, 1, wt_u3, u3b,
+                                         u3a, (size_t)32 * HW2, 1, t, 20);
+      convT_q_k<32, 16, 1, true, 64, 80>
+          <<<dim3(80), 256, 0, stream>>>(u3a, (size_t)32 * HW2, 1, r3, r3Sz, TR,
+                                         wt_u2, u2b, u2a, (size_t)16 * HW1, 1, t, 80);
+      up1out_k<<<dim3(320), 256, 0, stream>>>(
           u2a, (size_t)16 * HW1, 1, r2, r2Sz, TR, r1, r1Sz, TR,
-          u1w, u1b, ow, ob, dout, t);
+          wt_u1, u1b, ow, ob, dout, t, 320);
     }
   }
 
   if (tier == 0) {
-    convT_b_k<64, 32, 4, 2, false><<<dim3(5, 4, 2 * TD), 256, 0, stream>>>(
-        r4, r4Sz, 48, r4, 0, 1, u3w, u3b, u3a, (size_t)32 * HW2, 48, H3, W3, 0);
-    convT_b_k<32, 16, 4, 1, true><<<dim3(10, 8, TD), 256, 0, stream>>>(
-        u3a, (size_t)32 * HW2, 48, r3, r3Sz, 48, u2w, u2b, u2a, (size_t)16 * HW1, 48,
-        H2, W2, 0);
-    up1out_k<<<dim3(20, 16, TD), 256, 0, stream>>>(
+    convT_q_k<64, 32, 2, false, 32, 40>
+        <<<dim3(960), 256, 0, stream>>>(r4, r4Sz, 48, r4, 0, 1, wt_u3, u3b,
+                                        u3a, (size_t)32 * HW2, 48, 0, 960);
+    convT_q_k<32, 16, 1, true, 64, 80>
+        <<<dim3(3840), 256, 0, stream>>>(u3a, (size_t)32 * HW2, 48, r3, r3Sz, 48,
+                                         wt_u2, u2b, u2a, (size_t)16 * HW1, 48, 0, 3840);
+    up1out_k<<<dim3(15360), 256, 0, stream>>>(
         u2a, (size_t)16 * HW1, 48, r2, r2Sz, 48, r1, r1Sz, 48,
-        u1w, u1b, ow, ob, dout, 0);
-  }
-}
+        wt_u1, u1b, ow, ob, dout, 0, 15360);
+  }
+}
```

After: 9.838 ms. +7.4%, slower.
